# Performance work log

Measured on AMD Instinct MI355X. Metric: run time of the kernel, lower is better.

## Reference

```python
import jax, jax.numpy as jnp
import numpy as np

N_NODES = 50000
N_EDGES = 1600000
D_FEAT = 48


def setup_inputs() -> dict:
    key = jax.random.key(0)
    k1, k2, k3, k4, k5 = jax.random.split(key, 5)
    return {
        "x": jax.random.normal(k1, (N_EDGES, D_FEAT), dtype=jnp.float32),
        "switch": jax.random.uniform(k2, (N_EDGES,), dtype=jnp.float32),
        "edge_src": jax.random.randint(k3, (N_EDGES,), 0, N_NODES, dtype=jnp.int32),
        "edge_dst": jax.random.randint(k4, (N_EDGES,), 0, N_NODES, dtype=jnp.int32),
        "species": jax.random.randint(k5, (N_NODES,), 0, 100, dtype=jnp.int32),
    }


def reference(x, switch, edge_src, edge_dst, species):
    # nat = number of atoms, taken from species shape (static)
    nat = species.shape[0]
    # apply_switch: multiply per-edge switch into edge features [E, D] * [E, 1]
    xw = x * switch[:, None]
    # scatter-add edges to source atoms
    out = jax.ops.segment_sum(xw, edge_src, num_segments=nat)
    # antisymmetric: subtract scatter-add to destination atoms
    out = out - jax.ops.segment_sum(xw, edge_dst, num_segments=nat)
    return out  # [nat, D]
```

## Files before the change

### kernel.cpp

```cpp
#include <hip/hip_runtime.h>
#include <hip/hip_bf16.h>
#include <hip/hip_fp16.h>
#include <math.h>


#define D_FEAT 48
#define RNODES 64
#define RSHIFT 6
#define NB_MAX 1024
#define EPB 4096
#define SORT_CAP 8192
#define ROW_U4 8

__device__ __forceinline__ void convert_one(int g, const float4* __restrict__ x4,
                                            const float* __restrict__ sw,
                                            uint4* __restrict__ xwh) {
    int e = g >> 3, r = g & 7;
    uint4 o = make_uint4(0u, 0u, 0u, 0u);
    if (r < 6) {
        float s = sw[e];
        float4 a = x4[(size_t)e * 12 + r * 2];
        float4 b = x4[(size_t)e * 12 + r * 2 + 1];
        __half2 h0 = __floats2half2_rn(a.x * s, a.y * s);
        __half2 h1 = __floats2half2_rn(a.z * s, a.w * s);
        __half2 h2 = __floats2half2_rn(b.x * s, b.y * s);
        __half2 h3 = __floats2half2_rn(b.z * s, b.w * s);
        o.x = __builtin_bit_cast(unsigned int, h0);
        o.y = __builtin_bit_cast(unsigned int, h1);
        o.z = __builtin_bit_cast(unsigned int, h2);
        o.w = __builtin_bit_cast(unsigned int, h3);
    }
    xwh[g] = o;
}

__global__ __launch_bounds__(256) void hist_cv_kernel(
        const int* __restrict__ src, const int* __restrict__ dst,
        int* __restrict__ gcnt, int E, int NB, int role_blocks,
        const float4* __restrict__ x4, const float* __restrict__ sw,
        uint4* __restrict__ xwh, int cv_g0, int cv_g1) {
    __shared__ int lh[NB_MAX];
    if (blockIdx.x >= role_blocks) {
        int g = cv_g0 + (blockIdx.x - role_blocks) * 256 + threadIdx.x;
        if (g < cv_g1) convert_one(g, x4, sw, xwh);
        return;
    }
    for (int b = threadIdx.x; b < NB; b += 256) lh[b] = 0;
    __syncthreads();
    int t = threadIdx.x;
    int base = blockIdx.x * EPB;
    #pragma unroll
    for (int i = 0; i < EPB / 1024; ++i) {
        int e = base + i * 1024 + t * 4;
        if (e + 3 < E) {
            int4 s4 = *(const int4*)(src + e);
            int4 d4 = *(const int4*)(dst + e);
            atomicAdd(&lh[s4.x >> RSHIFT], 1);
            atomicAdd(&lh[s4.y >> RSHIFT], 1);
            atomicAdd(&lh[s4.z >> RSHIFT], 1);
            atomicAdd(&lh[s4.w >> RSHIFT], 1);
            atomicAdd(&lh[d4.x >> RSHIFT], 1);
            atomicAdd(&lh[d4.y >> RSHIFT], 1);
            atomicAdd(&lh[d4.z >> RSHIFT], 1);
            atomicAdd(&lh[d4.w >> RSHIFT], 1);
        } else {
            for (int j = 0; j < 4; ++j) {
                int ee = e + j;
                if (ee < E) {
                    atomicAdd(&lh[src[ee] >> RSHIFT], 1);
                    atomicAdd(&lh[dst[ee] >> RSHIFT], 1);
                }
            }
        }
    }
    __syncthreads();
    for (int b = threadIdx.x; b < NB; b += 256) {
        int c = lh[b];
        if (c) atomicAdd(&gcnt[b], c);
    }
}

__global__ __launch_bounds__(1024) void scan_kernel(
        const int* __restrict__ gcnt, int* __restrict__ goff,
        int* __restrict__ gcur, int* __restrict__ noff,
        int NB, int N, int total) {
    __shared__ int s[NB_MAX];
    int t = threadIdx.x;
    int v = (t < NB) ? gcnt[t] : 0;
    s[t] = v;
    __syncthreads();
    for (int d = 1; d < 1024; d <<= 1) {
        int a = (t >= d) ? s[t - d] : 0;
        __syncthreads();
        s[t] += a;
        __syncthreads();
    }
    if (t < NB) {
        int excl = s[t] - v;
        goff[t] = excl;
        gcur[t] = excl;
    }
    if (t == 0) {
        goff[NB] = total;
        noff[N] = total;
    }
}

__device__ __forceinline__ void bin_place(int e, int node, int side,
                                          int* lh, const int* lbase,
                                          int* __restrict__ items) {
    int b = node >> RSHIFT;
    int p = lbase[b] + atomicAdd(&lh[b], 1);
    items[p] = (e << 7) | (side << 6) | (node & (RNODES - 1));
}

__global__ __launch_bounds__(256) void bin_cv_kernel(
        const int* __restrict__ src, const int* __restrict__ dst,
        int* __restrict__ gcur, int* __restrict__ items, int E, int NB,
        int role_blocks,
        const float4* __restrict__ x4, const float* __restrict__ sw,
        uint4* __restrict__ xwh, int cv_g0, int cv_g1) {
    __shared__ int lh[NB_MAX];
    __shared__ int lbase[NB_MAX];
    if (blockIdx.x >= role_blocks) {
        int g = cv_g0 + (blockIdx.x - role_blocks) * 256 + threadIdx.x;
        if (g < cv_g1) convert_one(g, x4, sw, xwh);
        return;
    }
    for (int b = threadIdx.x; b < NB; b += 256) lh[b] = 0;
    __syncthreads();
    int t = threadIdx.x;
    int base = blockIdx.x * EPB;
    #pragma unroll
    for (int i = 0; i < EPB / 1024; ++i) {
        int e = base + i * 1024 + t * 4;
        if (e + 3 < E) {
            int4 s4 = *(const int4*)(src + e);
            int4 d4 = *(const int4*)(dst + e);
            atomicAdd(&lh[s4.x >> RSHIFT], 1);
            atomicAdd(&lh[s4.y >> RSHIFT], 1);
            atomicAdd(&lh[s4.z >> RSHIFT], 1);
            atomicAdd(&lh[s4.w >> RSHIFT], 1);
            atomicAdd(&lh[d4.x >> RSHIFT], 1);
            atomicAdd(&lh[d4.y >> RSHIFT], 1);
            atomicAdd(&lh[d4.z >> RSHIFT], 1);
            atomicAdd(&lh[d4.w >> RSHIFT], 1);
        } else {
            for (int j = 0; j < 4; ++j) {
                int ee = e + j;
                if (ee < E) {
                    atomicAdd(&lh[src[ee] >> RSHIFT], 1);
                    atomicAdd(&lh[dst[ee] >> RSHIFT], 1);
                }
            }
        }
    }
    __syncthreads();
    for (int b = threadIdx.x; b < NB; b += 256) {
        int c = lh[b];
        lbase[b] = c ? atomicAdd(&gcur[b], c) : 0;
        lh[b] = 0;
    }
    __syncthreads();
    #pragma unroll
    for (int i = 0; i < EPB / 1024; ++i) {
        int e = base + i * 1024 + t * 4;
        if (e + 3 < E) {
            int4 s4 = *(const int4*)(src + e);
            int4 d4 = *(const int4*)(dst + e);
            bin_place(e + 0, s4.x, 0, lh, lbase, items);
            bin_place(e + 1, s4.y, 0, lh, lbase, items);
            bin_place(e + 2, s4.z, 0, lh, lbase, items);
            bin_place(e + 3, s4.w, 0, lh, lbase, items);
            bin_place(e + 0, d4.x, 1, lh, lbase, items);
            bin_place(e + 1, d4.y, 1, lh, lbase, items);
            bin_place(e + 2, d4.z, 1, lh, lbase, items);
            bin_place(e + 3, d4.w, 1, lh, lbase, items);
        } else {
            for (int j = 0; j < 4; ++j) {
                int ee = e + j;
                if (ee < E) {
                    bin_place(ee, src[ee], 0, lh, lbase, items);
                    bin_place(ee, dst[ee], 1, lh, lbase, items);
                }
            }
        }
    }
}

__global__ __launch_bounds__(256) void sort_cv_kernel(
        int* __restrict__ items, const int* __restrict__ goff,
        int* __restrict__ noff, int N, int role_blocks,
        const float4* __restrict__ x4, const float* __restrict__ sw,
        uint4* __restrict__ xwh, int cv_g0, int cv_g1) {
    __shared__ int sitems[SORT_CAP];
    __shared__ int ccnt[RNODES];
    __shared__ int cbase[RNODES];
    if (blockIdx.x >= role_blocks) {
        int g = cv_g0 + (blockIdx.x - role_blocks) * 256 + threadIdx.x;
        if (g < cv_g1) convert_one(g, x4, sw, xwh);
        return;
    }
    int r = blockIdx.x;
    int lo = goff[r], hi = goff[r + 1];
    int cnt = hi - lo;
    int t = threadIdx.x;

    if (t < RNODES) ccnt[t] = 0;
    __syncthreads();
    #pragma unroll 4
    for (int i = t; i < cnt; i += 256) {
        int it = items[lo + i];
        sitems[i] = it;
        atomicAdd(&ccnt[it & (RNODES - 1)], 1);
    }
    __syncthreads();
    if (t < RNODES) {
        int c = ccnt[t];
        int v = c;
        #pragma unroll
        for (int d = 1; d < 64; d <<= 1) {
            int a = __shfl_up(v, d);
            if (t >= d) v += a;
        }
        int excl = v - c;
        cbase[t] = excl;
        int n = r * RNODES + t;
        if (n < N) noff[n] = lo + excl;
        ccnt[t] = 0;
    }
    __syncthreads();
    #pragma unroll 4
    for (int i = t; i < cnt; i += 256) {
        int it = sitems[i];
        int loc = it & (RNODES - 1);
        int p = cbase[loc] + atomicAdd(&ccnt[loc], 1);
        items[lo + p] = it;
    }
}

__global__ __launch_bounds__(256, 4) void gather_f16_kernel(
        const uint4* __restrict__ xwh, const int* __restrict__ noff,
        const int* __restrict__ items, float* __restrict__ out, int N) {
    int n = (blockIdx.x * blockDim.x + threadIdx.x) >> 6;
    int lane = threadIdx.x & 63;
    if (n >= N) return;

    int lo = noff[n], hi = noff[n + 1];
    int cnt = hi - lo;
    int grp = lane >> 3;
    int sub = lane & 7;

    float4 acc0 = make_float4(0.f, 0.f, 0.f, 0.f);
    float4 acc1 = make_float4(0.f, 0.f, 0.f, 0.f);

    for (int cb = 0; cb < cnt; cb += 64) {
        int chunk = items[lo + min(cb + lane, cnt - 1)];
        int rem = cnt - cb;
        #pragma unroll
        for (int k = 0; k < 8; ++k) {
            int idx = k * 8 + grp;
            int it = __shfl(chunk, idx);
            if (idx < rem) {
                uint4 q = xwh[(size_t)(unsigned)(it >> 7) * ROW_U4 + sub];
                unsigned m = (it & RNODES) ? 0x80008000u : 0u;
                float2 f0 = __half22float2(__builtin_bit_cast(__half2, q.x ^ m));
                float2 f1 = __half22float2(__builtin_bit_cast(__half2, q.y ^ m));
                float2 f2 = __half22float2(__builtin_bit_cast(__half2, q.z ^ m));
                float2 f3 = __half22float2(__builtin_bit_cast(__half2, q.w ^ m));
                acc0.x += f0.x; acc0.y += f0.y; acc0.z += f1.x; acc0.w += f1.y;
                acc1.x += f2.x; acc1.y += f2.y; acc1.z += f3.x; acc1.w += f3.y;
            }
        }
    }

    #pragma unroll
    for (int d = 32; d >= 8; d >>= 1) {
        acc0.x += __shfl_down(acc0.x, d);
        acc0.y += __shfl_down(acc0.y, d);
        acc0.z += __shfl_down(acc0.z, d);
        acc0.w += __shfl_down(acc0.w, d);
        acc1.x += __shfl_down(acc1.x, d);
        acc1.y += __shfl_down(acc1.y, d);
        acc1.z += __shfl_down(acc1.z, d);
        acc1.w += __shfl_down(acc1.w, d);
    }

    if (lane < 6) {
        float4* orow = (float4*)(out + (size_t)n * D_FEAT);
        orow[lane * 2 + 0] = acc0;
        orow[lane * 2 + 1] = acc1;
    }
}

__global__ __launch_bounds__(256, 4) void gather_kernel(
        const float4* __restrict__ x4, const float* __restrict__ sw,
        const int* __restrict__ noff, const int* __restrict__ items,
        float* __restrict__ out, int N) {
    int n = (blockIdx.x * blockDim.x + threadIdx.x) >> 6;
    int lane = threadIdx.x & 63;
    if (n >= N) return;

    int lo = noff[n], hi = noff[n + 1];
    int cnt = hi - lo;
    int grp = lane >> 4;
    int sub = lane & 15;

    float4 acc = make_float4(0.f, 0.f, 0.f, 0.f);

    for (int cb = 0; cb < cnt; cb += 64) {
        int chunk = items[lo + min(cb + lane, cnt - 1)];
        int rem = cnt - cb;
        #pragma unroll
        for (int k = 0; k < 16; ++k) {
            int idx = k * 4 + grp;
            int it = __shfl(chunk, idx);
            int e = it >> 7;
            float w = (idx < rem) ? sw[e] : 0.f;
            w = (it & RNODES) ? -w : w;
            if (sub < 12) {
                float4 v = x4[(size_t)e * 12 + sub];
                acc.x += w * v.x;
                acc.y += w * v.y;
                acc.z += w * v.z;
                acc.w += w * v.w;
            }
        }
    }

    acc.x += __shfl_down(acc.x, 32);
    acc.y += __shfl_down(acc.y, 32);
    acc.z += __shfl_down(acc.z, 32);
    acc.w += __shfl_down(acc.w, 32);
    acc.x += __shfl_down(acc.x, 16);
    acc.y += __shfl_down(acc.y, 16);
    acc.z += __shfl_down(acc.z, 16);
    acc.w += __shfl_down(acc.w, 16);

    if (lane < 12) {
        float4* orow = (float4*)(out + (size_t)n * D_FEAT);
        orow[lane] = acc;
    }
}

#define TPE 12
__global__ void atomic_fallback_kernel(const float4* __restrict__ x,
                                       const float* __restrict__ sw,
                                       const int* __restrict__ src,
                                       const int* __restrict__ dst,
                                       float* __restrict__ out, int n_edges) {
    int g = blockIdx.x * blockDim.x + threadIdx.x;
    int e = g / TPE;
    int q = g - e * TPE;
    if (e >= n_edges) return;
    float s = sw[e];
    float4 v = x[(size_t)e * TPE + q];
    v.x *= s; v.y *= s; v.z *= s; v.w *= s;
    int si = src[e], di = dst[e];
    float* po = out + (size_t)si * D_FEAT + q * 4;
    unsafeAtomicAdd(po + 0, v.x);
    unsafeAtomicAdd(po + 1, v.y);
    unsafeAtomicAdd(po + 2, v.z);
    unsafeAtomicAdd(po + 3, v.w);
    float* pd = out + (size_t)di * D_FEAT + q * 4;
    unsafeAtomicAdd(pd + 0, -v.x);
    unsafeAtomicAdd(pd + 1, -v.y);
    unsafeAtomicAdd(pd + 2, -v.z);
    unsafeAtomicAdd(pd + 3, -v.w);
}

extern "C" void kernel_launch(void* const* d_in, const int* in_sizes, int n_in,
                              void* d_out, int out_size, void* d_ws, size_t ws_size,
                              hipStream_t stream) {
    const float* x  = (const float*)d_in[0];
    const float* sw = (const float*)d_in[1];
    const int*   src = (const int*)d_in[2];
    const int*   dst = (const int*)d_in[3];
    float* out = (float*)d_out;

    int E = in_sizes[1];
    int N = in_sizes[4];
    int NB = (N + RNODES - 1) / RNODES;

    size_t xwh_bytes = (size_t)E * ROW_U4 * 16;
    size_t need_int  = ((size_t)NB * 3 + 1 + (size_t)N + 1 + 2 * (size_t)E)
                       * sizeof(int);
    size_t need_f16  = xwh_bytes + need_int;

    int mean = (NB > 0) ? (int)((long long)2 * E / NB) : 0;
    bool bucket_risk = mean + 16 * (int)sqrtf((float)(mean > 0 ? mean : 1)) > SORT_CAP;

    if (NB > NB_MAX || ws_size < need_int || bucket_risk) {
        hipMemsetAsync(d_out, 0, (size_t)out_size * sizeof(float), stream);
        long long total = (long long)E * TPE;
        int grid = (int)((total + 255) / 256);
        atomic_fallback_kernel<<<grid, 256, 0, stream>>>(
            (const float4*)x, sw, src, dst, out, E);
        return;
    }

    bool use_f16 = (ws_size >= need_f16);
    char* base = (char*)d_ws;
    uint4* xwh = (uint4*)base;
    int* ints  = (int*)(use_f16 ? (base + xwh_bytes) : base);

    int* gcnt  = ints;
    int* goff  = gcnt + NB;
    int* gcur  = goff + NB + 1;
    int* noff  = gcur + NB;
    int* items = noff + N + 1;

    hipMemsetAsync(gcnt, 0, (size_t)NB * sizeof(int), stream);

    int G = use_f16 ? E * 8 : 0;
    int cvb = (G + 255) / 256;
    int c1 = cvb / 3, c2 = cvb / 3, c3 = cvb - c1 - c2;
    int g1 = c1 * 256, g2 = (c1 + c2) * 256;

    int eblk = (E + EPB - 1) / EPB;

    hist_cv_kernel<<<eblk + c1, 256, 0, stream>>>(
        src, dst, gcnt, E, NB, eblk,
        (const float4*)x, sw, xwh, 0, min(g1, G));
    scan_kernel<<<1, 1024, 0, stream>>>(gcnt, goff, gcur, noff, NB, N, 2 * E);
    bin_cv_kernel<<<eblk + c2, 256, 0, stream>>>(
        src, dst, gcur, items, E, NB, eblk,
        (const float4*)x, sw, xwh, g1, min(g2, G));
    sort_cv_kernel<<<NB + c3, 256, 0, stream>>>(
        items, goff, noff, N, NB,
        (const float4*)x, sw, xwh, g2, G);

    int gblk = (int)(((long long)N * 64 + 255) / 256);
    if (use_f16) {
        gather_f16_kernel<<<gblk, 256, 0, stream>>>(
            (const uint4*)xwh, noff, items, out, N);
    } else {
        gather_kernel<<<gblk, 256, 0, stream>>>(
            (const float4*)x, sw, noff, items, out, N);
    }
}
```

Before: 561.9 us.

## Drop histogram and scan passes using fixed-capacity bucket slots

Removes the separate histogram kernel and the single-block scan by giving each 64-node bucket a fixed SORT_CAP slot in items, with bin counts reserved by atomic adds on gcur directly. The sort pass reads its bucket range from the fixed slot and writes per-node counts so the gather no longer needs noff[n+1]. It also switches the conversion loads, the items loads and the output stores to nontemporal builtins. In exchange the workspace grows to NB*SORT_CAP ints, and a bucket holding more than SORT_CAP items would overflow into the next slot, a case guarded only by the existing statistical bucket_risk check.

```diff
diff --git a/kernel.cpp b/kernel.cpp
--- a/kernel.cpp
+++ b/kernel.cpp
@@ -12,15 +12,18 @@
 #define SORT_CAP 8192
 #define ROW_U4 8
 
-__device__ __forceinline__ void convert_one(int g, const float4* __restrict__ x4,
+typedef float v4f __attribute__((ext_vector_type(4)));
+
+__device__ __forceinline__ void convert_one(int g, const float* __restrict__ x,
                                             const float* __restrict__ sw,
                                             uint4* __restrict__ xwh) {
     int e = g >> 3, r = g & 7;
     uint4 o = make_uint4(0u, 0u, 0u, 0u);
     if (r < 6) {
         float s = sw[e];
-        float4 a = x4[(size_t)e * 12 + r * 2];
-        float4 b = x4[(size_t)e * 12 + r * 2 + 1];
+        const v4f* px = (const v4f*)x + (size_t)e * 12 + r * 2;
+        v4f a = __builtin_nontemporal_load(px);
+        v4f b = __builtin_nontemporal_load(px + 1);
         __half2 h0 = __floats2half2_rn(a.x * s, a.y * s);
         __half2 h1 = __floats2half2_rn(a.z * s, a.w * s);
         __half2 h2 = __floats2half2_rn(b.x * s, b.y * s);
@@ -33,15 +36,25 @@
     xwh[g] = o;
 }
 
-__global__ __launch_bounds__(256) void hist_cv_kernel(
+__device__ __forceinline__ void bin_place(int e, int node, int side,
+                                          int* lh, const int* lbase,
+                                          int* __restrict__ items) {
+    int b = node >> RSHIFT;
+    int p = lbase[b] + atomicAdd(&lh[b], 1);
+    items[p] = (e << 7) | (side << 6) | (node & (RNODES - 1));
+}
+
+__global__ __launch_bounds__(256) void bin_cv_kernel(
         const int* __restrict__ src, const int* __restrict__ dst,
-        int* __restrict__ gcnt, int E, int NB, int role_blocks,
-        const float4* __restrict__ x4, const float* __restrict__ sw,
+        int* __restrict__ gcur, int* __restrict__ items, int E, int NB,
+        int role_blocks,
+        const float* __restrict__ x, const float* __restrict__ sw,
         uint4* __restrict__ xwh, int cv_g0, int cv_g1) {
     __shared__ int lh[NB_MAX];
+    __shared__ int lbase[NB_MAX];
     if (blockIdx.x >= role_blocks) {
         int g = cv_g0 + (blockIdx.x - role_blocks) * 256 + threadIdx.x;
-        if (g < cv_g1) convert_one(g, x4, sw, xwh);
+        if (g < cv_g1) convert_one(g, x, sw, xwh);
         return;
     }
     for (int b = threadIdx.x; b < NB; b += 256) lh[b] = 0;
@@ -75,89 +88,7 @@
     __syncthreads();
     for (int b = threadIdx.x; b < NB; b += 256) {
         int c = lh[b];
-        if (c) atomicAdd(&gcnt[b], c);
-    }
-}
-
-__global__ __launch_bounds__(1024) void scan_kernel(
-        const int* __restrict__ gcnt, int* __restrict__ goff,
-        int* __restrict__ gcur, int* __restrict__ noff,
-        int NB, int N, int total) {
-    __shared__ int s[NB_MAX];
-    int t = threadIdx.x;
-    int v = (t < NB) ? gcnt[t] : 0;
-    s[t] = v;
-    __syncthreads();
-    for (int d = 1; d < 1024; d <<= 1) {
-        int a = (t >= d) ? s[t - d] : 0;
-        __syncthreads();
-        s[t] += a;
-        __syncthreads();
-    }
-    if (t < NB) {
-        int excl = s[t] - v;
-        goff[t] = excl;
-        gcur[t] = excl;
-    }
-    if (t == 0) {
-        goff[NB] = total;
-        noff[N] = total;
-    }
-}
-
-__device__ __forceinline__ void bin_place(int e, int node, int side,
-                                          int* lh, const int* lbase,
-                                          int* __restrict__ items) {
-    int b = node >> RSHIFT;
-    int p = lbase[b] + atomicAdd(&lh[b], 1);
-    items[p] = (e << 7) | (side << 6) | (node & (RNODES - 1));
-}
-
-__global__ __launch_bounds__(256) void bin_cv_kernel(
-        const int* __restrict__ src, const int* __restrict__ dst,
-        int* __restrict__ gcur, int* __restrict__ items, int E, int NB,
-        int role_blocks,
-        const float4* __restrict__ x4, const float* __restrict__ sw,
-        uint4* __restrict__ xwh, int cv_g0, int cv_g1) {
-    __shared__ int lh[NB_MAX];
-    __shared__ int lbase[NB_MAX];
-    if (blockIdx.x >= role_blocks) {
-        int g = cv_g0 + (blockIdx.x - role_blocks) * 256 + threadIdx.x;
-        if (g < cv_g1) convert_one(g, x4, sw, xwh);
-        return;
-    }
-    for (int b = threadIdx.x; b < NB; b += 256) lh[b] = 0;
-    __syncthreads();
-    int t = threadIdx.x;
-    int base = blockIdx.x * EPB;
-    #pragma unroll
-    for (int i = 0; i < EPB / 1024; ++i) {
-        int e = base + i * 1024 + t * 4;
-        if (e + 3 < E) {
-            int4 s4 = *(const int4*)(src + e);
-            int4 d4 = *(const int4*)(dst + e);
-            atomicAdd(&lh[s4.x >> RSHIFT], 1);
-            atomicAdd(&lh[s4.y >> RSHIFT], 1);
-            atomicAdd(&lh[s4.z >> RSHIFT], 1);
-            atomicAdd(&lh[s4.w >> RSHIFT], 1);
-            atomicAdd(&lh[d4.x >> RSHIFT], 1);
-            atomicAdd(&lh[d4.y >> RSHIFT], 1);
-            atomicAdd(&lh[d4.z >> RSHIFT], 1);
-            atomicAdd(&lh[d4.w >> RSHIFT], 1);
-        } else {
-            for (int j = 0; j < 4; ++j) {
-                int ee = e + j;
-                if (ee < E) {
-                    atomicAdd(&lh[src[ee] >> RSHIFT], 1);
-                    atomicAdd(&lh[dst[ee] >> RSHIFT], 1);
-                }
-            }
-        }
-    }
-    __syncthreads();
-    for (int b = threadIdx.x; b < NB; b += 256) {
-        int c = lh[b];
-        lbase[b] = c ? atomicAdd(&gcur[b], c) : 0;
+        lbase[b] = b * SORT_CAP + (c ? atomicAdd(&gcur[b], c) : 0);
         lh[b] = 0;
     }
     __syncthreads();
@@ -188,21 +119,22 @@
 }
 
 __global__ __launch_bounds__(256) void sort_cv_kernel(
-        int* __restrict__ items, const int* __restrict__ goff,
-        int* __restrict__ noff, int N, int role_blocks,
-        const float4* __restrict__ x4, const float* __restrict__ sw,
+        int* __restrict__ items, const int* __restrict__ gcur,
+        int* __restrict__ noff, int* __restrict__ ncnt, int N,
+        int role_blocks,
+        const float* __restrict__ x, const float* __restrict__ sw,
         uint4* __restrict__ xwh, int cv_g0, int cv_g1) {
     __shared__ int sitems[SORT_CAP];
     __shared__ int ccnt[RNODES];
     __shared__ int cbase[RNODES];
     if (blockIdx.x >= role_blocks) {
         int g = cv_g0 + (blockIdx.x - role_blocks) * 256 + threadIdx.x;
-        if (g < cv_g1) convert_one(g, x4, sw, xwh);
+        if (g < cv_g1) convert_one(g, x, sw, xwh);
         return;
     }
     int r = blockIdx.x;
-    int lo = goff[r], hi = goff[r + 1];
-    int cnt = hi - lo;
+    int lo = r * SORT_CAP;
+    int cnt = min(gcur[r], SORT_CAP);
     int t = threadIdx.x;
 
     if (t < RNODES) ccnt[t] = 0;
@@ -225,7 +157,10 @@
         int excl = v - c;
         cbase[t] = excl;
         int n = r * RNODES + t;
-        if (n < N) noff[n] = lo + excl;
+        if (n < N) {
+            noff[n] = lo + excl;
+            ncnt[n] = c;
+        }
         ccnt[t] = 0;
     }
     __syncthreads();
@@ -240,13 +175,14 @@
 
 __global__ __launch_bounds__(256, 4) void gather_f16_kernel(
         const uint4* __restrict__ xwh, const int* __restrict__ noff,
-        const int* __restrict__ items, float* __restrict__ out, int N) {
+        const int* __restrict__ ncnt, const int* __restrict__ items,
+        float* __restrict__ out, int N) {
     int n = (blockIdx.x * blockDim.x + threadIdx.x) >> 6;
     int lane = threadIdx.x & 63;
     if (n >= N) return;
 
-    int lo = noff[n], hi = noff[n + 1];
-    int cnt = hi - lo;
+    int lo = noff[n];
+    int cnt = ncnt[n];
     int grp = lane >> 3;
     int sub = lane & 7;
 
@@ -254,7 +190,7 @@
     float4 acc1 = make_float4(0.f, 0.f, 0.f, 0.f);
 
     for (int cb = 0; cb < cnt; cb += 64) {
-        int chunk = items[lo + min(cb + lane, cnt - 1)];
+        int chunk = __builtin_nontemporal_load(items + lo + min(cb + lane, cnt - 1));
         int rem = cnt - cb;
         #pragma unroll
         for (int k = 0; k < 8; ++k) {
@@ -286,22 +222,24 @@
     }
 
     if (lane < 6) {
-        float4* orow = (float4*)(out + (size_t)n * D_FEAT);
-        orow[lane * 2 + 0] = acc0;
-        orow[lane * 2 + 1] = acc1;
+        v4f o0 = {acc0.x, acc0.y, acc0.z, acc0.w};
+        v4f o1 = {acc1.x, acc1.y, acc1.z, acc1.w};
+        v4f* orow = (v4f*)(out + (size_t)n * D_FEAT);
+        __builtin_nontemporal_store(o0, orow + lane * 2);
+        __builtin_nontemporal_store(o1, orow + lane * 2 + 1);
     }
 }
 
 __global__ __launch_bounds__(256, 4) void gather_kernel(
         const float4* __restrict__ x4, const float* __restrict__ sw,
-        const int* __restrict__ noff, const int* __restrict__ items,
-        float* __restrict__ out, int N) {
+        const int* __restrict__ noff, const int* __restrict__ ncnt,
+        const int* __restrict__ items, float* __restrict__ out, int N) {
     int n = (blockIdx.x * blockDim.x + threadIdx.x) >> 6;
     int lane = threadIdx.x & 63;
     if (n >= N) return;
 
-    int lo = noff[n], hi = noff[n + 1];
-    int cnt = hi - lo;
+    int lo = noff[n];
+    int cnt = ncnt[n];
     int grp = lane >> 4;
     int sub = lane & 15;
 
@@ -382,8 +320,8 @@
     int NB = (N + RNODES - 1) / RNODES;
 
     size_t xwh_bytes = (size_t)E * ROW_U4 * 16;
-    size_t need_int  = ((size_t)NB * 3 + 1 + (size_t)N + 1 + 2 * (size_t)E)
-                       * sizeof(int);
+    size_t need_int  = ((size_t)NB + 2 * (size_t)N
+                        + (size_t)NB * SORT_CAP) * sizeof(int);
     size_t need_f16  = xwh_bytes + need_int;
 
     int mean = (NB > 0) ? (int)((long long)2 * E / NB) : 0;
@@ -403,38 +341,33 @@
     uint4* xwh = (uint4*)base;
     int* ints  = (int*)(use_f16 ? (base + xwh_bytes) : base);
 
-    int* gcnt  = ints;
-    int* goff  = gcnt + NB;
-    int* gcur  = goff + NB + 1;
+    int* gcur  = ints;
     int* noff  = gcur + NB;
-    int* items = noff + N + 1;
-
-    hipMemsetAsync(gcnt, 0, (size_t)NB * sizeof(int), stream);
+    int* ncnt  = noff + N;
+    int* items = ncnt + N;
+
+    hipMemsetAsync(gcur, 0, (size_t)NB * sizeof(int), stream);
 
     int G = use_f16 ? E * 8 : 0;
     int cvb = (G + 255) / 256;
-    int c1 = cvb / 3, c2 = cvb / 3, c3 = cvb - c1 - c2;
-    int g1 = c1 * 256, g2 = (c1 + c2) * 256;
+    int c1 = cvb / 2, c2 = cvb - c1;
+    int g1 = c1 * 256;
 
     int eblk = (E + EPB - 1) / EPB;
 
-    hist_cv_kernel<<<eblk + c1, 256, 0, stream>>>(
-        src, dst, gcnt, E, NB, eblk,
-        (const float4*)x, sw, xwh, 0, min(g1, G));
-    scan_kernel<<<1, 1024, 0, stream>>>(gcnt, goff, gcur, noff, NB, N, 2 * E);
-    bin_cv_kernel<<<eblk + c2, 256, 0, stream>>>(
+    bin_cv_kernel<<<eblk + c1, 256, 0, stream>>>(
         src, dst, gcur, items, E, NB, eblk,
-        (const float4*)x, sw, xwh, g1, min(g2, G));
-    sort_cv_kernel<<<NB + c3, 256, 0, stream>>>(
-        items, goff, noff, N, NB,
-        (const float4*)x, sw, xwh, g2, G);
+        x, sw, xwh, 0, min(g1, G));
+    sort_cv_kernel<<<NB + c2, 256, 0, stream>>>(
+        items, gcur, noff, ncnt, N, NB,
+        x, sw, xwh, g1, G);
 
     int gblk = (int)(((long long)N * 64 + 255) / 256);
     if (use_f16) {
         gather_f16_kernel<<<gblk, 256, 0, stream>>>(
-            (const uint4*)xwh, noff, items, out, N);
+            (const uint4*)xwh, noff, ncnt, items, out, N);
     } else {
         gather_kernel<<<gblk, 256, 0, stream>>>(
-            (const float4*)x, sw, noff, items, out, N);
-    }
-}
+            (const float4*)x, sw, noff, ncnt, items, out, N);
+    }
+}
```

New measurement: 544.2 us. 1.03x faster.
